# Optimization experiments

Hardware: AMD Instinct MI355X
Metric: run time of the kernel (lower is better)

## Reference

```python
import jax, jax.numpy as jnp
import numpy as np

N_NODES = 50000
N_EDGES = 800000
IN_DIM = 128
E_FEATS = 64
H = 8
D = IN_DIM // H
NEG_SLOPE = 0.2


def setup_inputs() -> dict:
    key = jax.random.key(0)
    ks = jax.random.split(key, 9)
    h = jax.random.normal(ks[0], (N_NODES, IN_DIM), dtype=jnp.float32)
    edge_features = jax.random.normal(ks[1], (N_EDGES, E_FEATS), dtype=jnp.float32)
    src = jax.random.randint(ks[2], (N_EDGES,), 0, N_NODES, dtype=jnp.int32)
    dst = jax.random.randint(ks[3], (N_EDGES,), 0, N_NODES, dtype=jnp.int32)
    s = 0.05
    Wq = jax.random.normal(ks[4], (IN_DIM, IN_DIM), dtype=jnp.float32) * s
    Wk = jax.random.normal(ks[5], (IN_DIM, IN_DIM), dtype=jnp.float32) * s
    Wv = jax.random.normal(ks[6], (IN_DIM, IN_DIM), dtype=jnp.float32) * s
    We = jax.random.normal(ks[7], (H, E_FEATS), dtype=jnp.float32) * s
    Wres = jax.random.normal(ks[8], (IN_DIM, IN_DIM), dtype=jnp.float32) * s
    return {"h": h, "edge_features": edge_features, "src": src, "dst": dst,
            "Wq": Wq, "Wk": Wk, "Wv": Wv, "We": We, "Wres": Wres}


def reference(h, edge_features, src, dst, Wq, Wk, Wv, We, Wres):
    N = h.shape[0]
    # QKV projections (feat_drop is identity at eval)
    q = (h @ Wq.T).reshape(N, H, D)
    k = (h @ Wk.T).reshape(N, H, D)
    v = (h @ Wv.T).reshape(N, H, D)
    # ee / m_att are computed in the original forward but never used (dead code)
    _ee = edge_features @ We.T  # [E, H]

    # v_dot_u('q','k'): dot(q[dst], k[src]) per edge, per head -> [E, H]
    e = jnp.einsum('ehd,ehd->eh', q[dst], k[src])
    e = jnp.where(e >= 0, e, NEG_SLOPE * e)  # leaky_relu

    # edge_softmax over incoming edges of each destination node
    m = jax.ops.segment_max(e, dst, num_segments=N)          # [N, H]
    ex = jnp.exp(e - m[dst])                                 # [E, H]
    z = jax.ops.segment_sum(ex, dst, num_segments=N)         # [N, H]
    alpha = ex / z[dst]                                      # [E, H] (attn_drop identity)

    # weighted aggregation: sum_e alpha * v[src]
    msg = v[src] * alpha[:, :, None]                         # [E, H, D]
    rst = jax.ops.segment_sum(msg, dst, num_segments=N)      # [N, H, D]
    rst = rst.reshape(N, H * D)
    rst = rst + h @ Wres.T                                   # residual
    return rst
```

## Files before the change

### kernel.cpp

```cpp
#include <hip/hip_runtime.h>


#define NEG_SLOPE 0.2f

typedef __attribute__((ext_vector_type(8))) short short8;
typedef __attribute__((ext_vector_type(4))) float f32x4;

__device__ __forceinline__ unsigned short f2bf(float f) {
    unsigned int u = __builtin_bit_cast(unsigned int, f);
    u = (u + 0x7fffu + ((u >> 16) & 1u)) >> 16;
    return (unsigned short)u;
}
__device__ __forceinline__ float bf2f(unsigned short s) {
    unsigned int u = (unsigned int)s << 16;
    return __builtin_bit_cast(float, u);
}

__global__ __launch_bounds__(256) void zero_kernel(int* __restrict__ p, int n4)
{
    int t = blockIdx.x * 256 + threadIdx.x;
    if (t < n4) reinterpret_cast<int4*>(p)[t] = make_int4(0, 0, 0, 0);
}

__global__ __launch_bounds__(256) void wconv_kernel(
    const float* __restrict__ Wq, const float* __restrict__ Wk,
    const float* __restrict__ Wv, const float* __restrict__ Wres,
    unsigned short* __restrict__ wpk)
{
    int u = blockIdx.x * 256 + threadIdx.x;
    int l = u & 63;
    int v = u >> 6;
    int kk = v & 3;
    int wct = v >> 2;
    int ct = wct & 7;
    int w = wct >> 3;
    const float* W = (w == 0) ? Wq : (w == 1) ? Wk : (w == 2) ? Wv : Wres;
    const float* srcp = W + (size_t)(ct * 16 + (l & 15)) * 128 + kk * 32 + (l >> 4) * 8;
    float4 lo = *reinterpret_cast<const float4*>(srcp);
    float4 hi = *reinterpret_cast<const float4*>(srcp + 4);
    short8 o;
    o[0] = (short)f2bf(lo.x); o[1] = (short)f2bf(lo.y);
    o[2] = (short)f2bf(lo.z); o[3] = (short)f2bf(lo.w);
    o[4] = (short)f2bf(hi.x); o[5] = (short)f2bf(hi.y);
    o[6] = (short)f2bf(hi.z); o[7] = (short)f2bf(hi.w);
    *reinterpret_cast<short8*>(wpk + (size_t)u * 8) = o;
}

__global__ __launch_bounds__(256) void proj_mfma_kernel(
    const float* __restrict__ h,
    const unsigned short* __restrict__ wpk,
    float* __restrict__ q, unsigned short* __restrict__ kb,
    unsigned short* __restrict__ vb, float* __restrict__ res, int N)
{
    const int wid = threadIdx.x >> 6;
    const int lane = threadIdx.x & 63;
    const int row0 = blockIdx.x * 128 + wid * 32;
    const int r = lane & 15, g = lane >> 4;

    short8 afrag[2][4];
    #pragma unroll
    for (int grp = 0; grp < 2; ++grp) {
        int arow = row0 + grp * 16 + r;
        if (arow >= N) arow = N - 1;
        const float* hrow = h + (size_t)arow * 128 + g * 8;
        #pragma unroll
        for (int kk = 0; kk < 4; ++kk) {
            float4 lo = *reinterpret_cast<const float4*>(hrow + kk * 32);
            float4 hi = *reinterpret_cast<const float4*>(hrow + kk * 32 + 4);
            short8 a;
            a[0] = (short)f2bf(lo.x); a[1] = (short)f2bf(lo.y);
            a[2] = (short)f2bf(lo.z); a[3] = (short)f2bf(lo.w);
            a[4] = (short)f2bf(hi.x); a[5] = (short)f2bf(hi.y);
            a[6] = (short)f2bf(hi.z); a[7] = (short)f2bf(hi.w);
            afrag[grp][kk] = a;
        }
    }

    for (int w = 0; w < 4; ++w) {
        f32x4 acc[2][8];
        #pragma unroll
        for (int grp = 0; grp < 2; ++grp)
            #pragma unroll
            for (int ct = 0; ct < 8; ++ct) acc[grp][ct] = (f32x4)(0.f);

        #pragma unroll
        for (int ct = 0; ct < 8; ++ct) {
            const unsigned short* bp =
                wpk + ((size_t)((w * 8 + ct) * 4) * 64 + lane) * 8;
            short8 bfrag[4];
            #pragma unroll
            for (int kk = 0; kk < 4; ++kk)
                bfrag[kk] = *reinterpret_cast<const short8*>(bp + (size_t)kk * 512);
            #pragma unroll
            for (int grp = 0; grp < 2; ++grp)
                #pragma unroll
                for (int kk = 0; kk < 4; ++kk)
                    acc[grp][ct] = __builtin_amdgcn_mfma_f32_16x16x32_bf16(
                        afrag[grp][kk], bfrag[kk], acc[grp][ct], 0, 0, 0);
        }

        #pragma unroll
        for (int grp = 0; grp < 2; ++grp) {
            #pragma unroll
            for (int j = 0; j < 4; ++j) {
                int orow = row0 + grp * 16 + g * 4 + j;
                if (orow < N) {
                    if (w == 0) {
                        #pragma unroll
                        for (int ct = 0; ct < 8; ++ct)
                            q[(size_t)orow * 128 + ct * 16 + r] = acc[grp][ct][j];
                    } else if (w == 3) {
                        #pragma unroll
                        for (int ct = 0; ct < 8; ++ct)
                            res[(size_t)orow * 128 + ct * 16 + r] = acc[grp][ct][j];
                    } else {
                        unsigned short* O = (w == 1) ? kb : vb;
                        #pragma unroll
                        for (int ct = 0; ct < 8; ++ct)
                            O[(size_t)orow * 128 + ct * 16 + r] = f2bf(acc[grp][ct][j]);
                    }
                }
            }
        }
    }
}

__global__ __launch_bounds__(256) void count_kernel(
    const int* __restrict__ dst, int* __restrict__ cnt, int E)
{
    int e = blockIdx.x * 256 + threadIdx.x;
    if (e < E) atomicAdd(&cnt[dst[e]], 1);
}

__global__ __launch_bounds__(256) void blocksum_kernel(
    const int* __restrict__ cnt, int* __restrict__ bsum, int N)
{
    __shared__ int ws[4];
    const int tid = threadIdx.x;
    int base = blockIdx.x * 1024 + tid * 4;
    int s = 0;
    if (base + 3 < N) {
        int4 v = *reinterpret_cast<const int4*>(cnt + base);
        s = v.x + v.y + v.z + v.w;
    } else {
        for (int i = 0; i < 4; ++i)
            if (base + i < N) s += cnt[base + i];
    }
    #pragma unroll
    for (int m = 32; m >= 1; m >>= 1) s += __shfl_xor(s, m, 64);
    if ((tid & 63) == 0) ws[tid >> 6] = s;
    __syncthreads();
    if (tid == 0) bsum[blockIdx.x] = ws[0] + ws[1] + ws[2] + ws[3];
}

__global__ __launch_bounds__(64) void scanbsum_kernel(
    int* __restrict__ bsum, int NB)
{
    int lane = threadIdx.x;
    int v = (lane < NB) ? bsum[lane] : 0;
    #pragma unroll
    for (int off = 1; off < 64; off <<= 1) {
        int t = __shfl_up(v, off, 64);
        if (lane >= off) v += t;
    }
    int ex = __shfl_up(v, 1, 64);
    if (lane == 0) ex = 0;
    if (lane < NB) bsum[lane] = ex;
}

__global__ __launch_bounds__(256) void scanfinal_kernel(
    const int* __restrict__ cnt, const int* __restrict__ boff,
    int* __restrict__ row_start, int* __restrict__ cursor, int N, int E)
{
    __shared__ int wsum[4];
    const int tid = threadIdx.x, lane = tid & 63, w = tid >> 6;
    int base = blockIdx.x * 1024 + tid * 4;
    int a0 = 0, a1 = 0, a2 = 0, a3 = 0;
    if (base + 3 < N) {
        int4 v = *reinterpret_cast<const int4*>(cnt + base);
        a0 = v.x; a1 = v.y; a2 = v.z; a3 = v.w;
    } else {
        if (base + 0 < N) a0 = cnt[base + 0];
        if (base + 1 < N) a1 = cnt[base + 1];
        if (base + 2 < N) a2 = cnt[base + 2];
        if (base + 3 < N) a3 = cnt[base + 3];
    }
    const int tsum = a0 + a1 + a2 + a3;
    int v = tsum;
    #pragma unroll
    for (int off = 1; off < 64; off <<= 1) {
        int t = __shfl_up(v, off, 64);
        if (lane >= off) v += t;
    }
    if (lane == 63) wsum[w] = v;
    __syncthreads();
    int woff = 0;
    for (int i = 0; i < w; ++i) woff += wsum[i];
    int run = boff[blockIdx.x] + woff + v - tsum;

    int r0 = run, r1 = run + a0, r2 = r1 + a1, r3 = r2 + a2;
    if (base + 3 < N) {
        int4 o = make_int4(r0, r1, r2, r3);
        *reinterpret_cast<int4*>(row_start + base) = o;
        *reinterpret_cast<int4*>(cursor + base) = o;
    } else {
        int rr[4] = {r0, r1, r2, r3};
        for (int i = 0; i < 4; ++i)
            if (base + i < N) { row_start[base + i] = rr[i]; cursor[base + i] = rr[i]; }
    }
    if (blockIdx.x == 0 && tid == 0) row_start[N] = E;
}

__global__ __launch_bounds__(256) void scatter_kernel(
    const int* __restrict__ src, const int* __restrict__ dst,
    int* __restrict__ cursor, int* __restrict__ csr_src, int E)
{
    int e = blockIdx.x * 256 + threadIdx.x;
    if (e < E) {
        int d = dst[e];
        int pos = atomicAdd(&cursor[d], 1);
        csr_src[pos] = src[e];
    }
}

__global__ __launch_bounds__(256) void fused_agg_kernel(
    const float* __restrict__ q, const unsigned short* __restrict__ kb,
    const unsigned short* __restrict__ vb, const int* __restrict__ row_start,
    const int* __restrict__ csr_src, float* __restrict__ rst, int N)
{
    const int lane = threadIdx.x & 63;
    const int node = blockIdx.x * 4 + (threadIdx.x >> 6);
    if (node >= N) return;

    const int beg = row_start[node];
    const int end = row_start[node + 1];

    const size_t base = (size_t)node * 128 + 2 * lane;
    const float2 qv = *reinterpret_cast<const float2*>(q + base);

    float acc0 = 0.f, acc1 = 0.f, z = 0.f;

    int p = beg;
    if ((end - beg) & 1) {
        const int s = csr_src[p++];
        const size_t off = (size_t)s * 128 + 2 * lane;
        ushort2 kraw = *reinterpret_cast<const ushort2*>(kb + off);
        ushort2 vraw = *reinterpret_cast<const ushort2*>(vb + off);
        float pA = qv.x * bf2f(kraw.x) + qv.y * bf2f(kraw.y);
        #pragma unroll
        for (int m = 4; m >= 1; m >>= 1) pA += __shfl_xor(pA, m, 64);
        float e = (pA >= 0.f) ? pA : NEG_SLOPE * pA;
        e = __expf(e);
        z += e;
        acc0 = fmaf(e, bf2f(vraw.x), acc0);
        acc1 = fmaf(e, bf2f(vraw.y), acc1);
    }

    for (; p < end; p += 2) {
        const int s0 = csr_src[p];
        const int s1 = csr_src[p + 1];
        const size_t o0 = (size_t)s0 * 128 + 2 * lane;
        const size_t o1 = (size_t)s1 * 128 + 2 * lane;
        ushort2 k0 = *reinterpret_cast<const ushort2*>(kb + o0);
        ushort2 v0 = *reinterpret_cast<const ushort2*>(vb + o0);
        ushort2 k1 = *reinterpret_cast<const ushort2*>(kb + o1);
        ushort2 v1 = *reinterpret_cast<const ushort2*>(vb + o1);
        float pA = qv.x * bf2f(k0.x) + qv.y * bf2f(k0.y);
        float pB = qv.x * bf2f(k1.x) + qv.y * bf2f(k1.y);
        #pragma unroll
        for (int m = 4; m >= 1; m >>= 1) {
            pA += __shfl_xor(pA, m, 64);
            pB += __shfl_xor(pB, m, 64);
        }
        float e0 = (pA >= 0.f) ? pA : NEG_SLOPE * pA;
        float e1 = (pB >= 0.f) ? pB : NEG_SLOPE * pB;
        e0 = __expf(e0);
        e1 = __expf(e1);
        z += e0 + e1;
        acc0 = fmaf(e0, bf2f(v0.x), acc0);
        acc1 = fmaf(e0, bf2f(v0.y), acc1);
        acc0 = fmaf(e1, bf2f(v1.x), acc0);
        acc1 = fmaf(e1, bf2f(v1.y), acc1);
    }

    float2 rv = *reinterpret_cast<const float2*>(rst + base);
    if (end > beg) {
        float inv = 1.f / z;
        rv.x = fmaf(acc0, inv, rv.x);
        rv.y = fmaf(acc1, inv, rv.y);
    }
    *reinterpret_cast<float2*>(rst + base) = rv;
}

extern "C" void kernel_launch(void* const* d_in, const int* in_sizes, int n_in,
                              void* d_out, int out_size, void* d_ws, size_t ws_size,
                              hipStream_t stream) {
    const float* h    = (const float*)d_in[0];
    const int*   src  = (const int*)d_in[2];
    const int*   dst  = (const int*)d_in[3];
    const float* Wq   = (const float*)d_in[4];
    const float* Wk   = (const float*)d_in[5];
    const float* Wv   = (const float*)d_in[6];
    const float* Wres = (const float*)d_in[8];
    float* rst = (float*)d_out;

    const int N = in_sizes[0] / 128;
    const int E = in_sizes[2];

    float*          q   = (float*)d_ws;
    unsigned short* kb  = (unsigned short*)(q + (size_t)N * 128);
    unsigned short* vb  = kb + (size_t)N * 128;
    unsigned short* wpk = vb + (size_t)N * 128;
    int* cnt       = (int*)(wpk + 4 * 16384);
    int* row_start = cnt + N;
    int* cursor    = row_start + (N + 1);
    int* csr_src   = cursor + N;
    int* bsum      = csr_src + E;

    const int NB = (N + 1023) / 1024;

    zero_kernel<<<(N / 4 + 255) / 256, 256, 0, stream>>>(cnt, N / 4);
    wconv_kernel<<<32, 256, 0, stream>>>(Wq, Wk, Wv, Wres, wpk);
    proj_mfma_kernel<<<(N + 127) / 128, 256, 0, stream>>>(h, wpk, q, kb, vb,
                                                          rst, N);
    count_kernel<<<(E + 255) / 256, 256, 0, stream>>>(dst, cnt, E);
    blocksum_kernel<<<NB, 256, 0, stream>>>(cnt, bsum, N);
    scanbsum_kernel<<<1, 64, 0, stream>>>(bsum, NB);
    scanfinal_kernel<<<NB, 256, 0, stream>>>(cnt, bsum, row_start, cursor, N, E);
    scatter_kernel<<<(E + 255) / 256, 256, 0, stream>>>(src, dst, cursor,
                                                        csr_src, E);
    fused_agg_kernel<<<(N + 3) / 4, 256, 0, stream>>>(q, kb, vb, row_start,
                                                      csr_src, rst, N);
}
```

Baseline: 197.6 us.

## Merge setup kernels, interleave K/V in bf16, store q as bf16, prefetch CSR indices

Zeroing is merged with weight conversion, and the degree count is merged into the projection launch as extra blocks. The separate bsum scan kernel is dropped because each scan block now sums the preceding block totals itself. K and V are interleaved per node into one bf16 buffer so the aggregation does one 8-byte gather per edge instead of two 4-byte gathers. q is stored in bf16 and the next source indices are prefetched in the loop. This cuts launches and gather traffic, at the cost of lower q precision and more complex indexing.

```diff
diff --git a/kernel.cpp b/kernel.cpp
--- a/kernel.cpp
+++ b/kernel.cpp
@@ -2,6 +2,7 @@
 
 
 #define NEG_SLOPE 0.2f
+#define CB 1024
 
 typedef __attribute__((ext_vector_type(8))) short short8;
 typedef __attribute__((ext_vector_type(4))) float f32x4;
@@ -16,42 +17,50 @@
     return __builtin_bit_cast(float, u);
 }
 
-__global__ __launch_bounds__(256) void zero_kernel(int* __restrict__ p, int n4)
-{
-    int t = blockIdx.x * 256 + threadIdx.x;
-    if (t < n4) reinterpret_cast<int4*>(p)[t] = make_int4(0, 0, 0, 0);
-}
-
-__global__ __launch_bounds__(256) void wconv_kernel(
+__global__ __launch_bounds__(256) void zero_wconv_kernel(
     const float* __restrict__ Wq, const float* __restrict__ Wk,
     const float* __restrict__ Wv, const float* __restrict__ Wres,
-    unsigned short* __restrict__ wpk)
-{
-    int u = blockIdx.x * 256 + threadIdx.x;
-    int l = u & 63;
-    int v = u >> 6;
-    int kk = v & 3;
-    int wct = v >> 2;
-    int ct = wct & 7;
-    int w = wct >> 3;
-    const float* W = (w == 0) ? Wq : (w == 1) ? Wk : (w == 2) ? Wv : Wres;
-    const float* srcp = W + (size_t)(ct * 16 + (l & 15)) * 128 + kk * 32 + (l >> 4) * 8;
-    float4 lo = *reinterpret_cast<const float4*>(srcp);
-    float4 hi = *reinterpret_cast<const float4*>(srcp + 4);
-    short8 o;
-    o[0] = (short)f2bf(lo.x); o[1] = (short)f2bf(lo.y);
-    o[2] = (short)f2bf(lo.z); o[3] = (short)f2bf(lo.w);
-    o[4] = (short)f2bf(hi.x); o[5] = (short)f2bf(hi.y);
-    o[6] = (short)f2bf(hi.z); o[7] = (short)f2bf(hi.w);
-    *reinterpret_cast<short8*>(wpk + (size_t)u * 8) = o;
-}
-
-__global__ __launch_bounds__(256) void proj_mfma_kernel(
+    unsigned short* __restrict__ wpk, int* __restrict__ cnt, int n4)
+{
+    int t = blockIdx.x * 256 + threadIdx.x;
+    if (t < 8192) {
+        int l = t & 63;
+        int v = t >> 6;
+        int kk = v & 3;
+        int wct = v >> 2;
+        int ct = wct & 7;
+        int w = wct >> 3;
+        const float* W = (w == 0) ? Wq : (w == 1) ? Wk : (w == 2) ? Wv : Wres;
+        const float* srcp = W + (size_t)(ct * 16 + (l & 15)) * 128 + kk * 32 + (l >> 4) * 8;
+        float4 lo = *reinterpret_cast<const float4*>(srcp);
+        float4 hi = *reinterpret_cast<const float4*>(srcp + 4);
+        short8 o;
+        o[0] = (short)f2bf(lo.x); o[1] = (short)f2bf(lo.y);
+        o[2] = (short)f2bf(lo.z); o[3] = (short)f2bf(lo.w);
+        o[4] = (short)f2bf(hi.x); o[5] = (short)f2bf(hi.y);
+        o[6] = (short)f2bf(hi.z); o[7] = (short)f2bf(hi.w);
+        *reinterpret_cast<short8*>(wpk + (size_t)t * 8) = o;
+    } else {
+        int u = t - 8192;
+        if (u < n4) reinterpret_cast<int4*>(cnt)[u] = make_int4(0, 0, 0, 0);
+    }
+}
+
+__global__ __launch_bounds__(256) void proj_count_kernel(
     const float* __restrict__ h,
     const unsigned short* __restrict__ wpk,
-    float* __restrict__ q, unsigned short* __restrict__ kb,
-    unsigned short* __restrict__ vb, float* __restrict__ res, int N)
-{
+    unsigned short* __restrict__ qb, unsigned short* __restrict__ kvb,
+    float* __restrict__ res,
+    const int* __restrict__ dst, int* __restrict__ cnt,
+    int N, int E, int PB)
+{
+    if (blockIdx.x >= PB) {
+        int start = (blockIdx.x - PB) * 256 + threadIdx.x;
+        for (int e = start; e < E; e += CB * 256)
+            atomicAdd(&cnt[dst[e]], 1);
+        return;
+    }
+
     const int wid = threadIdx.x >> 6;
     const int lane = threadIdx.x & 63;
     const int row0 = blockIdx.x * 128 + wid * 32;
@@ -108,28 +117,23 @@
                     if (w == 0) {
                         #pragma unroll
                         for (int ct = 0; ct < 8; ++ct)
-                            q[(size_t)orow * 128 + ct * 16 + r] = acc[grp][ct][j];
+                            qb[(size_t)orow * 128 + ct * 16 + r] = f2bf(acc[grp][ct][j]);
                     } else if (w == 3) {
                         #pragma unroll
                         for (int ct = 0; ct < 8; ++ct)
                             res[(size_t)orow * 128 + ct * 16 + r] = acc[grp][ct][j];
                     } else {
-                        unsigned short* O = (w == 1) ? kb : vb;
+                        const int voff = (w == 2) ? 2 : 0;
                         #pragma unroll
-                        for (int ct = 0; ct < 8; ++ct)
-                            O[(size_t)orow * 128 + ct * 16 + r] = f2bf(acc[grp][ct][j]);
+                        for (int ct = 0; ct < 8; ++ct) {
+                            int idx = ct * 32 + 4 * (r >> 1) + (r & 1) + voff;
+                            kvb[(size_t)orow * 256 + idx] = f2bf(acc[grp][ct][j]);
+                        }
                     }
                 }
             }
         }
     }
-}
-
-__global__ __launch_bounds__(256) void count_kernel(
-    const int* __restrict__ dst, int* __restrict__ cnt, int E)
-{
-    int e = blockIdx.x * 256 + threadIdx.x;
-    if (e < E) atomicAdd(&cnt[dst[e]], 1);
 }
 
 __global__ __launch_bounds__(256) void blocksum_kernel(
@@ -153,27 +157,23 @@
     if (tid == 0) bsum[blockIdx.x] = ws[0] + ws[1] + ws[2] + ws[3];
 }
 
-__global__ __launch_bounds__(64) void scanbsum_kernel(
-    int* __restrict__ bsum, int NB)
-{
-    int lane = threadIdx.x;
-    int v = (lane < NB) ? bsum[lane] : 0;
-    #pragma unroll
-    for (int off = 1; off < 64; off <<= 1) {
-        int t = __shfl_up(v, off, 64);
-        if (lane >= off) v += t;
-    }
-    int ex = __shfl_up(v, 1, 64);
-    if (lane == 0) ex = 0;
-    if (lane < NB) bsum[lane] = ex;
-}
-
 __global__ __launch_bounds__(256) void scanfinal_kernel(
-    const int* __restrict__ cnt, const int* __restrict__ boff,
-    int* __restrict__ row_start, int* __restrict__ cursor, int N, int E)
-{
+    const int* __restrict__ cnt, const int* __restrict__ bsum,
+    int* __restrict__ row_start, int* __restrict__ cursor,
+    int N, int E, int NB)
+{
+    __shared__ int sboff;
     __shared__ int wsum[4];
     const int tid = threadIdx.x, lane = tid & 63, w = tid >> 6;
+
+    if (tid < 64) {
+        int v = (tid < NB && tid < blockIdx.x) ? bsum[tid] : 0;
+        #pragma unroll
+        for (int m = 32; m >= 1; m >>= 1) v += __shfl_xor(v, m, 64);
+        if (tid == 0) sboff = v;
+    }
+    __syncthreads();
+
     int base = blockIdx.x * 1024 + tid * 4;
     int a0 = 0, a1 = 0, a2 = 0, a3 = 0;
     if (base + 3 < N) {
@@ -196,7 +196,7 @@
     __syncthreads();
     int woff = 0;
     for (int i = 0; i < w; ++i) woff += wsum[i];
-    int run = boff[blockIdx.x] + woff + v - tsum;
+    int run = sboff + woff + v - tsum;
 
     int r0 = run, r1 = run + a0, r2 = r1 + a1, r3 = r2 + a2;
     if (base + 3 < N) {
@@ -224,9 +224,10 @@
 }
 
 __global__ __launch_bounds__(256) void fused_agg_kernel(
-    const float* __restrict__ q, const unsigned short* __restrict__ kb,
-    const unsigned short* __restrict__ vb, const int* __restrict__ row_start,
-    const int* __restrict__ csr_src, float* __restrict__ rst, int N)
+    const unsigned short* __restrict__ qb,
+    const unsigned short* __restrict__ kvb,
+    const int* __restrict__ row_start, const int* __restrict__ csr_src,
+    float* __restrict__ rst, int N)
 {
     const int lane = threadIdx.x & 63;
     const int node = blockIdx.x * 4 + (threadIdx.x >> 6);
@@ -234,39 +235,29 @@
 
     const int beg = row_start[node];
     const int end = row_start[node + 1];
-
-    const size_t base = (size_t)node * 128 + 2 * lane;
-    const float2 qv = *reinterpret_cast<const float2*>(q + base);
+    const int nE = end - beg;
+    const int* cp = csr_src + beg;
+
+    ushort2 qraw = *reinterpret_cast<const ushort2*>(qb + (size_t)node * 128 + 2 * lane);
+    const float qx = bf2f(qraw.x), qy = bf2f(qraw.y);
 
     float acc0 = 0.f, acc1 = 0.f, z = 0.f;
 
-    int p = beg;
-    if ((end - beg) & 1) {
-        const int s = csr_src[p++];
-        const size_t off = (size_t)s * 128 + 2 * lane;
-        ushort2 kraw = *reinterpret_cast<const ushort2*>(kb + off);
-        ushort2 vraw = *reinterpret_cast<const ushort2*>(vb + off);
-        float pA = qv.x * bf2f(kraw.x) + qv.y * bf2f(kraw.y);
-        #pragma unroll
-        for (int m = 4; m >= 1; m >>= 1) pA += __shfl_xor(pA, m, 64);
-        float e = (pA >= 0.f) ? pA : NEG_SLOPE * pA;
-        e = __expf(e);
-        z += e;
-        acc0 = fmaf(e, bf2f(vraw.x), acc0);
-        acc1 = fmaf(e, bf2f(vraw.y), acc1);
-    }
-
-    for (; p < end; p += 2) {
-        const int s0 = csr_src[p];
-        const int s1 = csr_src[p + 1];
-        const size_t o0 = (size_t)s0 * 128 + 2 * lane;
-        const size_t o1 = (size_t)s1 * 128 + 2 * lane;
-        ushort2 k0 = *reinterpret_cast<const ushort2*>(kb + o0);
-        ushort2 v0 = *reinterpret_cast<const ushort2*>(vb + o0);
-        ushort2 k1 = *reinterpret_cast<const ushort2*>(kb + o1);
-        ushort2 v1 = *reinterpret_cast<const ushort2*>(vb + o1);
-        float pA = qv.x * bf2f(k0.x) + qv.y * bf2f(k0.y);
-        float pB = qv.x * bf2f(k1.x) + qv.y * bf2f(k1.y);
+    int i = 0;
+    int sa = (nE > 0) ? cp[0] : 0;
+    int sb = (nE > 1) ? cp[1] : 0;
+
+    while (i + 2 <= nE) {
+        const int s0 = sa, s1 = sb;
+        i += 2;
+        if (i < nE)     sa = cp[i];
+        if (i + 1 < nE) sb = cp[i + 1];
+
+        ushort4 kv0 = *reinterpret_cast<const ushort4*>(kvb + (size_t)s0 * 256 + 4 * lane);
+        ushort4 kv1 = *reinterpret_cast<const ushort4*>(kvb + (size_t)s1 * 256 + 4 * lane);
+
+        float pA = qx * bf2f(kv0.x) + qy * bf2f(kv0.y);
+        float pB = qx * bf2f(kv1.x) + qy * bf2f(kv1.y);
         #pragma unroll
         for (int m = 4; m >= 1; m >>= 1) {
             pA += __shfl_xor(pA, m, 64);
@@ -277,14 +268,26 @@
         e0 = __expf(e0);
         e1 = __expf(e1);
         z += e0 + e1;
-        acc0 = fmaf(e0, bf2f(v0.x), acc0);
-        acc1 = fmaf(e0, bf2f(v0.y), acc1);
-        acc0 = fmaf(e1, bf2f(v1.x), acc0);
-        acc1 = fmaf(e1, bf2f(v1.y), acc1);
-    }
-
+        acc0 = fmaf(e0, bf2f(kv0.z), acc0);
+        acc1 = fmaf(e0, bf2f(kv0.w), acc1);
+        acc0 = fmaf(e1, bf2f(kv1.z), acc0);
+        acc1 = fmaf(e1, bf2f(kv1.w), acc1);
+    }
+    if (i < nE) {
+        ushort4 kv0 = *reinterpret_cast<const ushort4*>(kvb + (size_t)sa * 256 + 4 * lane);
+        float pA = qx * bf2f(kv0.x) + qy * bf2f(kv0.y);
+        #pragma unroll
+        for (int m = 4; m >= 1; m >>= 1) pA += __shfl_xor(pA, m, 64);
+        float e0 = (pA >= 0.f) ? pA : NEG_SLOPE * pA;
+        e0 = __expf(e0);
+        z += e0;
+        acc0 = fmaf(e0, bf2f(kv0.z), acc0);
+        acc1 = fmaf(e0, bf2f(kv0.w), acc1);
+    }
+
+    const size_t base = (size_t)node * 128 + 2 * lane;
     float2 rv = *reinterpret_cast<const float2*>(rst + base);
-    if (end > beg) {
+    if (nE > 0) {
         float inv = 1.f / z;
         rv.x = fmaf(acc0, inv, rv.x);
         rv.y = fmaf(acc1, inv, rv.y);
@@ -307,28 +310,28 @@
     const int N = in_sizes[0] / 128;
     const int E = in_sizes[2];
 
-    float*          q   = (float*)d_ws;
-    unsigned short* kb  = (unsigned short*)(q + (size_t)N * 128);
-    unsigned short* vb  = kb + (size_t)N * 128;
-    unsigned short* wpk = vb + (size_t)N * 128;
+    unsigned short* qb  = (unsigned short*)d_ws;
+    unsigned short* kvb = qb + (size_t)N * 128;
+    unsigned short* wpk = kvb + (size_t)N * 256;
     int* cnt       = (int*)(wpk + 4 * 16384);
     int* row_start = cnt + N;
     int* cursor    = row_start + (N + 1);
     int* csr_src   = cursor + N;
     int* bsum      = csr_src + E;
 
+    const int n4 = N / 4;
     const int NB = (N + 1023) / 1024;
-
-    zero_kernel<<<(N / 4 + 255) / 256, 256, 0, stream>>>(cnt, N / 4);
-    wconv_kernel<<<32, 256, 0, stream>>>(Wq, Wk, Wv, Wres, wpk);
-    proj_mfma_kernel<<<(N + 127) / 128, 256, 0, stream>>>(h, wpk, q, kb, vb,
-                                                          rst, N);
-    count_kernel<<<(E + 255) / 256, 256, 0, stream>>>(dst, cnt, E);
+    const int PB = (N + 127) / 128;
+
+    zero_wconv_kernel<<<(8192 + n4 + 255) / 256, 256, 0, stream>>>(
+        Wq, Wk, Wv, Wres, wpk, cnt, n4);
+    proj_count_kernel<<<PB + CB, 256, 0, stream>>>(h, wpk, qb, kvb, rst,
+                                                   dst, cnt, N, E, PB);
     blocksum_kernel<<<NB, 256, 0, stream>>>(cnt, bsum, N);
-    scanbsum_kernel<<<1, 64, 0, stream>>>(bsum, NB);
-    scanfinal_kernel<<<NB, 256, 0, stream>>>(cnt, bsum, row_start, cursor, N, E);
+    scanfinal_kernel<<<NB, 256, 0, stream>>>(cnt, bsum, row_start, cursor,
+                                             N, E, NB);
     scatter_kernel<<<(E + 255) / 256, 256, 0, stream>>>(src, dst, cursor,
                                                         csr_src, E);
-    fused_agg_kernel<<<(N + 3) / 4, 256, 0, stream>>>(q, kb, vb, row_start,
+    fused_agg_kernel<<<(N + 3) / 4, 256, 0, stream>>>(qb, kvb, row_start,
                                                       csr_src, rst, N);
 }
```

Measured after the change: 170.1 us. 1.16x faster.
